# Kernel tuning notes

Hardware: AMD Instinct MI355X
Metric: run time of the kernel (lower is better)

Reference implementation:

```python
import jax, jax.numpy as jnp
import numpy as np

# DoG parameters derived from init kwargs: sigma_low=1.0, truncate=4.0
SIGMA_LOW = 1.0
SIGMA_HIGH = 1.6  # sigma_low * 1.6
KSIZE_LOW = 9     # 2*ceil(4.0*1.0)+1
KSIZE_HIGH = 15   # 2*ceil(4.0*1.6)+1


def gaussian_kernel1d(ksize: int, sigma: float) -> jnp.ndarray:
    # Matches kornia's 1D gaussian: centered, normalized to sum 1.
    t = jnp.arange(ksize, dtype=jnp.float32) - (ksize - 1) / 2.0
    g = jnp.exp(-(t * t) / (2.0 * sigma * sigma))
    return g / jnp.sum(g)


def _conv1d_along_axis(x: jnp.ndarray, g: jnp.ndarray, axis: int) -> jnp.ndarray:
    # x: (B, C, D, H, W); depthwise 1D cross-correlation along `axis` with
    # replicate ('edge') boundary handling, as in kornia filter3d(border_type='replicate').
    C = x.shape[1]
    k = g.shape[0]
    pads = [(0, 0)] * 5
    pads[axis] = (k // 2, k // 2)
    xp = jnp.pad(x, pads, mode='edge')
    kshape = [1, 1, 1]
    kshape[axis - 2] = k
    w = jnp.tile(g.reshape(1, 1, *kshape), (C, 1, 1, 1, 1))  # (C,1,kd,kh,kw)
    return jax.lax.conv_general_dilated(
        xp, w, window_strides=(1, 1, 1), padding='VALID',
        dimension_numbers=('NCDHW', 'OIDHW', 'NCDHW'),
        feature_group_count=C)


def gaussian_blur3d(x: jnp.ndarray, sigma: float, ksize: int) -> jnp.ndarray:
    # The 3D kernel is an outer product of normalized 1D gaussians, so the
    # dense 3D convolution is exactly equal to three separable 1D passes.
    g = gaussian_kernel1d(ksize, sigma)
    for ax in (2, 3, 4):
        x = _conv1d_along_axis(x, g, ax)
    return x


def setup_inputs() -> dict:
    key = jax.random.key(0)
    x = jax.random.normal(key, (2, 1, 160, 160, 160), dtype=jnp.float32)
    return {"x": x}


def reference(x) -> jnp.ndarray:
    low_pass = gaussian_blur3d(x, SIGMA_LOW, KSIZE_LOW)
    high_pass = gaussian_blur3d(x, SIGMA_HIGH, KSIZE_HIGH)
    return low_pass - high_pass
```

## Files before the change

### kernel.cpp

```cpp
#include <hip/hip_runtime.h>
#include <math.h>

#define DIMS 160
#define PLANE (DIMS*DIMS)
#define NB 2
#define RH 7
#define RL 4
#define KH 15
#define KL 9
#define TSX 16
#define TSY 32
#define NTX (DIMS/TSX)
#define NTY (DIMS/TSY)
#define CZ 16
#define NCH (DIMS/CZ)
#define NSTEPS (CZ + 2*RH)
#define YHR (TSY + 2*RH)
#define YLR (TSY + 2*RL)
#define RAWSZ 1860
#define SH 50
#define SL 42
#define NBLK (NTX*NTY*NCH*NB)

struct DoGW { float gl[KL]; float gh[KH]; };

__device__ __forceinline__ int raw_off(int r) {
  const int x = r & 15;
  return r * 40 + ((8 * ((x >> 2) & 3) + (x & 3) - 8 * (x & 3)) & 31);
}

__global__ __launch_bounds__(512, 4)
void dog_v7(const float* __restrict__ X, float* __restrict__ out, DoGW w) {
  __shared__ float sRaw[2][RAWSZ];
  __shared__ float sXh[2][TSX * SH];
  __shared__ float sXl[2][TSX * SL];

  const int bid = blockIdx.x;
  const int xt = bid % NTX;
  const int yt = (bid / NTX) % NTY;
  const int zc = (bid / (NTX * NTY)) % NCH;
  const int b  = bid / (NTX * NTY * NCH);
  const int x0 = xt * TSX, y0 = yt * TSY, z0 = zc * CZ;
  const float* Xb = X + (size_t)b * DIMS * PLANE;
  const int tid = threadIdx.x;
  const bool xfast = (x0 >= 8) && (x0 + 24 <= DIMS);

  const bool l_on = tid < YHR * 8;
  const int lrow = tid >> 3, lq = tid & 7;
  const int lyg = min(max(y0 + lrow - RH, 0), DIMS - 1);
  const int lxb = x0 - 8 + 4 * lq;
  const int lof = raw_off(lrow) + 4 * lq;

  const bool x_on = tid < YHR * 4;
  const int xr = tid >> 2, xq = tid & 3;
  const int xof = raw_off(xr) + 4 * xq;
  const bool xlow = (xr >= 3) && (xr <= 42);

  const int cy = tid >> 4, cx = tid & 15;

  auto loadP = [&](int s, float4& v) {
    if (!l_on) return;
    const int zsrc = min(max(z0 - RH + s, 0), DIMS - 1);
    const float* rowp = Xb + ((size_t)zsrc * DIMS + lyg) * DIMS;
    if (xfast) {
      v = *(const float4*)(rowp + lxb);
    } else {
      v.x = rowp[min(max(lxb + 0, 0), DIMS - 1)];
      v.y = rowp[min(max(lxb + 1, 0), DIMS - 1)];
      v.z = rowp[min(max(lxb + 2, 0), DIMS - 1)];
      v.w = rowp[min(max(lxb + 3, 0), DIMS - 1)];
    }
  };
  auto stageP = [&](const float4& v, int buf) {
    if (!l_on) return;
    float* p = &sRaw[buf][lof];
    p[0] = v.x; p[1] = v.y; p[2] = v.z; p[3] = v.w;
  };

  float accH[KH], accL[KL + 3];
  #pragma unroll
  for (int i = 0; i < KH; ++i) accH[i] = 0.f;
  #pragma unroll
  for (int i = 0; i < KL + 3; ++i) accL[i] = 0.f;

  auto consumeQ = [&](int q) {
    const int qb = q & 1;
    float ph = 0.f, pl = 0.f;
    #pragma unroll
    for (int j = 0; j < KH; ++j) ph = fmaf(w.gh[j], sXh[qb][cx * SH + cy + j], ph);
    #pragma unroll
    for (int j = 0; j < KL; ++j) pl = fmaf(w.gl[j], sXl[qb][cx * SL + cy + j], pl);
    #pragma unroll
    for (int i = 0; i < KH; ++i) accH[i] = fmaf(w.gh[KH - 1 - i], ph, accH[i]);
    #pragma unroll
    for (int i = 3; i < KL + 3; ++i) accL[i] = fmaf(w.gl[KL + 2 - i], pl, accL[i]);
    if (q >= 2 * RH) {
      const int zo = z0 + q - 2 * RH;
      out[((size_t)(b * DIMS + zo) * DIMS + (y0 + cy)) * DIMS + (x0 + cx)] = accL[0] - accH[0];
    }
    #pragma unroll
    for (int i = 0; i < KH - 1; ++i) accH[i] = accH[i + 1];
    accH[KH - 1] = 0.f;
    #pragma unroll
    for (int i = 0; i < KL + 2; ++i) accL[i] = accL[i + 1];
    accL[KL + 2] = 0.f;
  };

  auto xconvP = [&](int cur) {
    if (!x_on) return;
    const float* p = &sRaw[cur][xof];
    float v[20];
    #pragma unroll
    for (int j = 0; j < 20; ++j) v[j] = p[j];
    #pragma unroll
    for (int c = 0; c < 4; ++c) {
      float a = 0.f;
      #pragma unroll
      for (int k = 0; k < KH; ++k) a = fmaf(w.gh[k], v[c + 1 + k], a);
      sXh[cur][(4 * xq + c) * SH + xr] = a;
    }
    if (xlow) {
      #pragma unroll
      for (int c = 0; c < 4; ++c) {
        float a = 0.f;
        #pragma unroll
        for (int k = 0; k < KL; ++k) a = fmaf(w.gl[k], v[c + 4 + k], a);
        sXl[cur][(4 * xq + c) * SL + (xr - 3)] = a;
      }
    }
  };

  float4 vH;
  {
    float4 v0;
    loadP(0, v0);
    stageP(v0, 0);
    loadP(1, vH);
  }
  __syncthreads();

  #pragma unroll 2
  for (int s = 0; s < NSTEPS; ++s) {
    const int cur = s & 1;
    if (s + 1 < NSTEPS) stageP(vH, 1 - cur);
    if (s + 2 < NSTEPS) loadP(s + 2, vH);
    if (s >= 1) consumeQ(s - 1);
    xconvP(cur);
    __syncthreads();
  }
  consumeQ(NSTEPS - 1);
}

extern "C" void kernel_launch(void* const* d_in, const int* in_sizes, int n_in,
                              void* d_out, int out_size, void* d_ws, size_t ws_size,
                              hipStream_t stream) {
  const float* X = (const float*)d_in[0];
  float* out = (float*)d_out;

  DoGW w;
  {
    double s = 0.0;
    for (int i = 0; i < KL; ++i) {
      double t = i - (KL - 1) / 2.0;
      double g = exp(-(t * t) / (2.0 * 1.0 * 1.0));
      w.gl[i] = (float)g; s += g;
    }
    for (int i = 0; i < KL; ++i) w.gl[i] = (float)((double)w.gl[i] / s);
    s = 0.0;
    for (int i = 0; i < KH; ++i) {
      double t = i - (KH - 1) / 2.0;
      double g = exp(-(t * t) / (2.0 * 1.6 * 1.6));
      w.gh[i] = (float)g; s += g;
    }
    for (int i = 0; i < KH; ++i) w.gh[i] = (float)((double)w.gh[i] / s);
  }

  dog_v7<<<NBLK, 512, 0, stream>>>(X, out, w);
}
```

Before: 134.6 us.

## Warp-specialize DoG kernel, two outputs per consumer thread, deeper z chunks

Splits the 512 threads into dedicated roles: 256 consumer threads each compute two y-outputs, a group of x-convolution threads, and a separate group of loader threads that fetch two float4s per row. Doubles the z chunk length to amortise the 14-plane halo, and replaces the swizzled shared layout with padded strides so loads and stores can be vectorised as float2 and float4. The intent is to cut halo recomputation and shared-memory instruction count, and to run load, x-conv and z-accumulate work concurrently. In exchange there are half as many blocks, each consumer thread holds twice the accumulator registers, and bank conflicts may come back with the plain padded layout.

Result: no change. 136.2 us (+1.2%).

```diff
diff --git a/kernel.cpp b/kernel.cpp
--- a/kernel.cpp
+++ b/kernel.cpp
@@ -12,28 +12,25 @@
 #define TSY 32
 #define NTX (DIMS/TSX)
 #define NTY (DIMS/TSY)
-#define CZ 16
+#define CZ 32
 #define NCH (DIMS/CZ)
 #define NSTEPS (CZ + 2*RH)
 #define YHR (TSY + 2*RH)
-#define YLR (TSY + 2*RL)
-#define RAWSZ 1860
-#define SH 50
-#define SL 42
+#define SR 40
+#define SH 52
+#define SL 44
+#define RAWSZ (YHR*SR)
+#define XHSZ (TSX*SH)
+#define XLSZ (TSX*SL)
 #define NBLK (NTX*NTY*NCH*NB)
 
 struct DoGW { float gl[KL]; float gh[KH]; };
 
-__device__ __forceinline__ int raw_off(int r) {
-  const int x = r & 15;
-  return r * 40 + ((8 * ((x >> 2) & 3) + (x & 3) - 8 * (x & 3)) & 31);
-}
-
 __global__ __launch_bounds__(512, 4)
-void dog_v7(const float* __restrict__ X, float* __restrict__ out, DoGW w) {
-  __shared__ float sRaw[2][RAWSZ];
-  __shared__ float sXh[2][TSX * SH];
-  __shared__ float sXl[2][TSX * SL];
+void dog_v8(const float* __restrict__ X, float* __restrict__ out, DoGW w) {
+  __shared__ __align__(16) float sRaw[2][RAWSZ];
+  __shared__ __align__(16) float sXh[2][XHSZ];
+  __shared__ __align__(16) float sXl[2][XLSZ];
 
   const int bid = blockIdx.x;
   const int xt = bid % NTX;
@@ -45,73 +42,109 @@
   const int tid = threadIdx.x;
   const bool xfast = (x0 >= 8) && (x0 + 24 <= DIMS);
 
-  const bool l_on = tid < YHR * 8;
-  const int lrow = tid >> 3, lq = tid & 7;
+  const bool y_on = tid < 256;
+  const int cx  = tid & 15;
+  const int cy0 = 2 * ((tid >> 4) & 15);
+  const int hb = cx * SH + cy0;
+  const int lb = cx * SL + cy0;
+  float* const obase = out + ((size_t)b * DIMS * PLANE) + (size_t)(y0 + cy0) * DIMS + (x0 + cx);
+
+  const bool x_on = (tid >= 256) && (tid < 256 + YHR * 4);
+  const int xu = tid - 256;
+  const int xr = xu >> 2, xq = xu & 3;
+
+  const bool l_on = tid >= (512 - YHR * 4);
+  const int lu = tid - (512 - YHR * 4);
+  const int lrow = lu >> 2, lt = lu & 3;
   const int lyg = min(max(y0 + lrow - RH, 0), DIMS - 1);
-  const int lxb = x0 - 8 + 4 * lq;
-  const int lof = raw_off(lrow) + 4 * lq;
-
-  const bool x_on = tid < YHR * 4;
-  const int xr = tid >> 2, xq = tid & 3;
-  const int xof = raw_off(xr) + 4 * xq;
-  const bool xlow = (xr >= 3) && (xr <= 42);
-
-  const int cy = tid >> 4, cx = tid & 15;
-
-  auto loadP = [&](int s, float4& v) {
-    if (!l_on) return;
+  const int lxb = x0 - 8 + 4 * lt;
+
+  float4 vA, vB;
+
+  auto loadP = [&](int s) {
     const int zsrc = min(max(z0 - RH + s, 0), DIMS - 1);
     const float* rowp = Xb + ((size_t)zsrc * DIMS + lyg) * DIMS;
     if (xfast) {
-      v = *(const float4*)(rowp + lxb);
+      vA = *(const float4*)(rowp + lxb);
+      vB = *(const float4*)(rowp + lxb + 16);
     } else {
-      v.x = rowp[min(max(lxb + 0, 0), DIMS - 1)];
-      v.y = rowp[min(max(lxb + 1, 0), DIMS - 1)];
-      v.z = rowp[min(max(lxb + 2, 0), DIMS - 1)];
-      v.w = rowp[min(max(lxb + 3, 0), DIMS - 1)];
-    }
-  };
-  auto stageP = [&](const float4& v, int buf) {
-    if (!l_on) return;
-    float* p = &sRaw[buf][lof];
-    p[0] = v.x; p[1] = v.y; p[2] = v.z; p[3] = v.w;
-  };
-
-  float accH[KH], accL[KL + 3];
+      vA.x = rowp[min(max(lxb + 0, 0), DIMS - 1)];
+      vA.y = rowp[min(max(lxb + 1, 0), DIMS - 1)];
+      vA.z = rowp[min(max(lxb + 2, 0), DIMS - 1)];
+      vA.w = rowp[min(max(lxb + 3, 0), DIMS - 1)];
+      vB.x = rowp[min(max(lxb + 16, 0), DIMS - 1)];
+      vB.y = rowp[min(max(lxb + 17, 0), DIMS - 1)];
+      vB.z = rowp[min(max(lxb + 18, 0), DIMS - 1)];
+      vB.w = rowp[min(max(lxb + 19, 0), DIMS - 1)];
+    }
+  };
+  auto stageP = [&](int buf) {
+    float* p = &sRaw[buf][lrow * SR + 4 * lt];
+    *(float4*)(p) = vA;
+    *(float4*)(p + 16) = vB;
+  };
+
+  float accH0[KH], accH1[KH], accL0[KL + 3], accL1[KL + 3];
   #pragma unroll
-  for (int i = 0; i < KH; ++i) accH[i] = 0.f;
+  for (int i = 0; i < KH; ++i) { accH0[i] = 0.f; accH1[i] = 0.f; }
   #pragma unroll
-  for (int i = 0; i < KL + 3; ++i) accL[i] = 0.f;
+  for (int i = 0; i < KL + 3; ++i) { accL0[i] = 0.f; accL1[i] = 0.f; }
 
   auto consumeQ = [&](int q) {
     const int qb = q & 1;
-    float ph = 0.f, pl = 0.f;
-    #pragma unroll
-    for (int j = 0; j < KH; ++j) ph = fmaf(w.gh[j], sXh[qb][cx * SH + cy + j], ph);
-    #pragma unroll
-    for (int j = 0; j < KL; ++j) pl = fmaf(w.gl[j], sXl[qb][cx * SL + cy + j], pl);
-    #pragma unroll
-    for (int i = 0; i < KH; ++i) accH[i] = fmaf(w.gh[KH - 1 - i], ph, accH[i]);
-    #pragma unroll
-    for (int i = 3; i < KL + 3; ++i) accL[i] = fmaf(w.gl[KL + 2 - i], pl, accL[i]);
+    float f[16], g[10];
+    #pragma unroll
+    for (int j = 0; j < 8; ++j) {
+      float2 t = *(const float2*)&sXh[qb][hb + 2 * j];
+      f[2 * j] = t.x; f[2 * j + 1] = t.y;
+    }
+    #pragma unroll
+    for (int j = 0; j < 5; ++j) {
+      float2 t = *(const float2*)&sXl[qb][lb + 2 * j];
+      g[2 * j] = t.x; g[2 * j + 1] = t.y;
+    }
+    float ph0 = 0.f, ph1 = 0.f, pl0 = 0.f, pl1 = 0.f;
+    #pragma unroll
+    for (int j = 0; j < KH; ++j) {
+      ph0 = fmaf(w.gh[j], f[j], ph0);
+      ph1 = fmaf(w.gh[j], f[j + 1], ph1);
+    }
+    #pragma unroll
+    for (int j = 0; j < KL; ++j) {
+      pl0 = fmaf(w.gl[j], g[j], pl0);
+      pl1 = fmaf(w.gl[j], g[j + 1], pl1);
+    }
+    #pragma unroll
+    for (int i = 0; i < KH; ++i) {
+      accH0[i] = fmaf(w.gh[KH - 1 - i], ph0, accH0[i]);
+      accH1[i] = fmaf(w.gh[KH - 1 - i], ph1, accH1[i]);
+    }
+    #pragma unroll
+    for (int i = 3; i < KL + 3; ++i) {
+      accL0[i] = fmaf(w.gl[KL + 2 - i], pl0, accL0[i]);
+      accL1[i] = fmaf(w.gl[KL + 2 - i], pl1, accL1[i]);
+    }
     if (q >= 2 * RH) {
-      const int zo = z0 + q - 2 * RH;
-      out[((size_t)(b * DIMS + zo) * DIMS + (y0 + cy)) * DIMS + (x0 + cx)] = accL[0] - accH[0];
-    }
-    #pragma unroll
-    for (int i = 0; i < KH - 1; ++i) accH[i] = accH[i + 1];
-    accH[KH - 1] = 0.f;
-    #pragma unroll
-    for (int i = 0; i < KL + 2; ++i) accL[i] = accL[i + 1];
-    accL[KL + 2] = 0.f;
+      float* op = obase + (size_t)(z0 + q - 2 * RH) * PLANE;
+      op[0]    = accL0[0] - accH0[0];
+      op[DIMS] = accL1[0] - accH1[0];
+    }
+    #pragma unroll
+    for (int i = 0; i < KH - 1; ++i) { accH0[i] = accH0[i + 1]; accH1[i] = accH1[i + 1]; }
+    accH0[KH - 1] = 0.f; accH1[KH - 1] = 0.f;
+    #pragma unroll
+    for (int i = 0; i < KL + 2; ++i) { accL0[i] = accL0[i + 1]; accL1[i] = accL1[i + 1]; }
+    accL0[KL + 2] = 0.f; accL1[KL + 2] = 0.f;
   };
 
   auto xconvP = [&](int cur) {
-    if (!x_on) return;
-    const float* p = &sRaw[cur][xof];
+    const float* p = &sRaw[cur][xr * SR + 4 * xq];
     float v[20];
     #pragma unroll
-    for (int j = 0; j < 20; ++j) v[j] = p[j];
+    for (int j = 0; j < 5; ++j) {
+      float4 t = *(const float4*)(p + 4 * j);
+      v[4 * j] = t.x; v[4 * j + 1] = t.y; v[4 * j + 2] = t.z; v[4 * j + 3] = t.w;
+    }
     #pragma unroll
     for (int c = 0; c < 4; ++c) {
       float a = 0.f;
@@ -119,7 +152,7 @@
       for (int k = 0; k < KH; ++k) a = fmaf(w.gh[k], v[c + 1 + k], a);
       sXh[cur][(4 * xq + c) * SH + xr] = a;
     }
-    if (xlow) {
+    if (xr >= 3 && xr <= 42) {
       #pragma unroll
       for (int c = 0; c < 4; ++c) {
         float a = 0.f;
@@ -130,25 +163,29 @@
     }
   };
 
-  float4 vH;
+  if (l_on) { loadP(0); stageP(0); loadP(1); }
+  __syncthreads();
+
+  for (int sb = 0; sb < NSTEPS - 1; sb += 5) {
+    #pragma unroll
+    for (int u = 0; u < 5; ++u) {
+      const int s = sb + u;
+      const int cur = s & 1;
+      if (l_on) {
+        if (s + 1 < NSTEPS) stageP(1 - cur);
+        if (s + 2 < NSTEPS) loadP(s + 2);
+      }
+      if (y_on && s >= 1) consumeQ(s - 1);
+      if (x_on) xconvP(cur);
+      __syncthreads();
+    }
+  }
   {
-    float4 v0;
-    loadP(0, v0);
-    stageP(v0, 0);
-    loadP(1, vH);
+    if (y_on) consumeQ(NSTEPS - 2);
+    if (x_on) xconvP((NSTEPS - 1) & 1);
+    __syncthreads();
+    if (y_on) consumeQ(NSTEPS - 1);
   }
-  __syncthreads();
-
-  #pragma unroll 2
-  for (int s = 0; s < NSTEPS; ++s) {
-    const int cur = s & 1;
-    if (s + 1 < NSTEPS) stageP(vH, 1 - cur);
-    if (s + 2 < NSTEPS) loadP(s + 2, vH);
-    if (s >= 1) consumeQ(s - 1);
-    xconvP(cur);
-    __syncthreads();
-  }
-  consumeQ(NSTEPS - 1);
 }
 
 extern "C" void kernel_launch(void* const* d_in, const int* in_sizes, int n_in,
@@ -175,5 +212,5 @@
     for (int i = 0; i < KH; ++i) w.gh[i] = (float)((double)w.gh[i] / s);
   }
 
-  dog_v7<<<NBLK, 512, 0, stream>>>(X, out, w);
+  dog_v8<<<NBLK, 512, 0, stream>>>(X, out, w);
 }
```
